# Optimization experiments

Hardware: AMD Instinct MI355X
Metric: run time of the kernel (lower is better)

Reference implementation:

```python
import jax, jax.numpy as jnp
import numpy as np

B, N, C = 4, 65536, 192
HEADS = 6
HEADC = C // HEADS
EPS = 1e-5


def _ln(x, w, b):
    # custom LayerNorm: unbiased std (ddof=1), divide by (std + eps)
    m = x.mean(-1, keepdims=True)
    s = jnp.std(x, axis=-1, keepdims=True, ddof=1)
    return w * ((x - m) / (s + EPS)) + b


def setup_inputs() -> dict:
    key = jax.random.key(0)
    ks = jax.random.split(key, 8)
    x = jax.random.normal(ks[0], (B, N, C), dtype=jnp.float32)
    # 1x1 conv weights == channel matmuls; [out_c, in_c]
    qkv_w = jax.random.normal(ks[1], (3 * C, C), dtype=jnp.float32) * 0.05
    qkv_b = jax.random.normal(ks[2], (3 * C,), dtype=jnp.float32) * 0.02
    o1_w = jax.random.normal(ks[3], (C, C), dtype=jnp.float32) * 0.05
    o1_b = jax.random.normal(ks[4], (C,), dtype=jnp.float32) * 0.02
    o2_w = jax.random.normal(ks[5], (C, C), dtype=jnp.float32) * 0.05
    o2_b = jax.random.normal(ks[6], (C,), dtype=jnp.float32) * 0.02
    kln_w = jnp.ones((HEADS, 1, HEADC), dtype=jnp.float32)
    kln_b = jnp.zeros((HEADS, 1, HEADC), dtype=jnp.float32)
    vln_w = jnp.ones((HEADS, 1, HEADC), dtype=jnp.float32)
    vln_b = jnp.zeros((HEADS, 1, HEADC), dtype=jnp.float32)
    return {"x": x, "qkv_w": qkv_w, "qkv_b": qkv_b, "o1_w": o1_w,
            "o1_b": o1_b, "o2_w": o2_w, "o2_b": o2_b,
            "kln_w": kln_w, "kln_b": kln_b, "vln_w": vln_w, "vln_b": vln_b,
            "H": 256, "W": 256}


def reference(x, qkv_w, qkv_b, o1_w, o1_b, o2_w, o2_b,
              kln_w, kln_b, vln_w, vln_b, H, W):
    b, n, c = x.shape
    heads, headc = kln_w.shape[0], kln_w.shape[-1]
    # 1x1 conv QKV projection (per-pixel linear)
    qkv = jnp.einsum('bnc,dc->bnd', x, qkv_w) + qkv_b          # [B,N,3C]
    qkv = qkv.reshape(b, n, heads, 3 * headc).transpose(0, 2, 1, 3)  # [B,h,N,3d]
    q, k, v = jnp.split(qkv, 3, axis=-1)                        # each [B,h,N,d]
    k = _ln(k, kln_w, kln_b)
    v = _ln(v, vln_w, vln_b)
    # Galerkin (softmax-free) linear attention
    kv = jnp.einsum('bhnd,bhne->bhde', k, v) / n                # [B,h,d,d]
    attn = jnp.einsum('bhnd,bhde->bhne', q, kv)                 # [B,h,N,d]
    attn = attn.transpose(0, 2, 1, 3).reshape(b, n, c)          # [B,N,C]
    ret = attn + x                                              # residual
    h = jax.nn.gelu(jnp.einsum('bnc,dc->bnd', ret, o1_w) + o1_b,
                    approximate=False)
    out = jnp.einsum('bnc,dc->bnd', h, o2_w) + o2_b + x
    return out
```

## Files before the change

### kernel.cpp

```cpp
#include <hip/hip_runtime.h>
#include <math.h>

typedef __attribute__((ext_vector_type(8)))  __bf16 bf16x8;
typedef __attribute__((ext_vector_type(16))) float  f32x16;
typedef __attribute__((ext_vector_type(4)))  float  f32x4;
typedef __attribute__((ext_vector_type(4)))  int    i32x4;
typedef __attribute__((ext_vector_type(4)))  unsigned u32x4;

union FR { bf16x8 v; u32x4 q; unsigned u[4]; };

__device__ inline f32x16 MF(bf16x8 a, bf16x8 b, f32x16 c) {
    return __builtin_amdgcn_mfma_f32_32x32x16_bf16(a, b, c, 0, 0, 0);
}
__device__ inline unsigned pk(float a, float b) {
    unsigned ua = (__builtin_bit_cast(unsigned, a) + 0x8000u) >> 16;
    unsigned ub = (__builtin_bit_cast(unsigned, b) + 0x8000u) >> 16;
    return ua | (ub << 16);
}
__device__ inline unsigned short bfr(float a) {
    return (unsigned short)((__builtin_bit_cast(unsigned, a) + 0x8000u) >> 16);
}
__device__ inline float ubf(unsigned short s) {
    return __builtin_bit_cast(float, (unsigned)s << 16);
}
__device__ inline float gelu_f(float g) {
    float z  = g * 0.70710678118654752f;
    float az = fabsf(z);
    float t  = 1.0f / (1.0f + 0.3275911f * az);
    float poly = t*(0.254829592f + t*(-0.284496736f + t*(1.421413741f +
                 t*(-1.453152027f + t*1.061405429f))));
    float er = 1.0f - poly * __expf(-az * az);
    er = (z < 0.f) ? -er : er;
    return 0.5f * g * (1.0f + er);
}

__global__ void k0_pack(const float* __restrict__ qkv_w, const float* __restrict__ qkv_b,
                        const float* __restrict__ o2w,
                        unsigned* __restrict__ wkvpk, unsigned* __restrict__ o2pk,
                        float* __restrict__ bkv)
{
    int idx = blockIdx.x * 256 + threadIdx.x;
    if (idx < 36864) {
        int kt = idx / 3072, r = idx % 3072, nt = r / 256, r3 = r % 256;
        int l = r3 >> 2, q = r3 & 3;
        int c  = kt * 16 + (l >> 5) * 8 + q * 2;
        int rp = nt * 32 + (l & 31);
        int row = (rp >> 6) * 96 + 32 + (rp & 63);
        wkvpk[idx] = pk(qkv_w[row * 192 + c], qkv_w[row * 192 + c + 1]);
    } else if (idx < 55296) {
        int i2 = idx - 36864;
        int kt = i2 / 1536, r = i2 % 1536, jt = r / 256, r3 = r % 256;
        int l = r3 >> 2, q = r3 & 3;
        int jj = kt * 16 + (l >> 5) * 8 + q * 2;
        int j  = jt * 32 + (l & 31);
        o2pk[i2] = pk(o2w[j * 192 + jj], o2w[j * 192 + jj + 1]);
    } else if (idx < 55680) {
        int rp = idx - 55296;
        bkv[rp] = qkv_b[(rp >> 6) * 96 + 32 + (rp & 63)];
    }
}

__global__ __launch_bounds__(256, 2)
void k1a(const float* __restrict__ x, const u32x4* __restrict__ Wpk,
         const float* __restrict__ bkv, u32x4* __restrict__ kvraw)
{
    const int tid = threadIdx.x;
    const int wid = tid >> 6, lane = tid & 63;
    const int col = lane & 31, lh = lane >> 5;
    const int w = blockIdx.x * 4 + wid;
    const int b = w >> 11, sp = w & 2047;

    const float* xr = x + ((long)(b * 65536 + sp * 32 + col)) * 192 + lh * 8;
    FR afr[12];
#pragma unroll
    for (int kt = 0; kt < 12; ++kt) {
        f32x4 a0 = *(const f32x4*)(xr + kt * 16);
        f32x4 a1 = *(const f32x4*)(xr + kt * 16 + 4);
        afr[kt].u[0] = pk(a0.x, a0.y); afr[kt].u[1] = pk(a0.z, a0.w);
        afr[kt].u[2] = pk(a1.x, a1.y); afr[kt].u[3] = pk(a1.z, a1.w);
    }
    float biasv[12];
#pragma unroll
    for (int nt = 0; nt < 12; ++nt) biasv[nt] = bkv[nt * 32 + col];

#pragma unroll
    for (int half = 0; half < 2; ++half) {
        f32x16 acc[6];
#pragma unroll
        for (int n = 0; n < 6; ++n) acc[n] = (f32x16)(biasv[half * 6 + n]);
#pragma unroll
        for (int kt = 0; kt < 12; ++kt) {
            bf16x8 av = afr[kt].v;
#pragma unroll
            for (int n = 0; n < 6; ++n) {
                FR bv; bv.q = Wpk[(kt * 12 + half * 6 + n) * 64 + lane];
                acc[n] = MF(av, bv.v, acc[n]);
            }
        }
#pragma unroll
        for (int n = 0; n < 6; ++n) {
            int nt = half * 6 + n;
            u32x4 lo, hi;
            lo.x = pk(acc[n][0],  acc[n][1]);  lo.y = pk(acc[n][2],  acc[n][3]);
            lo.z = pk(acc[n][4],  acc[n][5]);  lo.w = pk(acc[n][6],  acc[n][7]);
            hi.x = pk(acc[n][8],  acc[n][9]);  hi.y = pk(acc[n][10], acc[n][11]);
            hi.z = pk(acc[n][12], acc[n][13]); hi.w = pk(acc[n][14], acc[n][15]);
            long base = ((long)((b * 2048 + sp) * 12 + nt)) * 128 + lane * 2;
            kvraw[base] = lo; kvraw[base + 1] = hi;
        }
    }
}

__global__ __launch_bounds__(256, 2)
void k1b(const u32x4* __restrict__ kvraw,
         const float* __restrict__ klnw, const float* __restrict__ klnb,
         const float* __restrict__ vlnw, const float* __restrict__ vlnb,
         float* __restrict__ kvg)
{
    __shared__ __align__(16) unsigned short kvT[64 * 40];
    __shared__ float stats[4][64][2];
    __shared__ float smean[64], sinv[64];
    __shared__ float lnw_s[64], lnb_s[64];

    const int t = threadIdx.x;
    const int split = blockIdx.x, h = blockIdx.y, b = blockIdx.z;

    if (t < 32)      { lnw_s[t] = klnw[h * 32 + t];      lnb_s[t] = klnb[h * 32 + t]; }
    else if (t < 64) { lnw_s[t] = vlnw[h * 32 + t - 32]; lnb_s[t] = vlnb[h * 32 + t - 32]; }

    const int lane = t & 63;
    const int col = lane & 31, lh = lane >> 5;
    const int nt  = 2 * h + (t >> 7);
    const int l   = (t & 127) >> 1;
    const int rh  = (t & 1) * 8;
    const int chw = (t >> 7) * 32 + (l & 31);
    const int p0  = 4 * (l >> 5) + rh * 2;
    const int c64 = t & 63, pp = c64 & 31, kvh = c64 >> 5, qq = t >> 6;

    f32x16 kvacc = (f32x16)(0.0f);

    for (int c = 0; c < 32; ++c) {
        int sp = split * 32 + c;
        __syncthreads();
        u32x4 d = kvraw[((long)((b * 2048 + sp) * 12 + nt)) * 128 + l * 2 + (t & 1)];
        *(uint2*)&kvT[chw * 40 + p0]     = make_uint2(d.x, d.y);
        *(uint2*)&kvT[chw * 40 + p0 + 8] = make_uint2(d.z, d.w);
        __syncthreads();
        float vals[8]; float s = 0.f, s2 = 0.f;
#pragma unroll
        for (int i = 0; i < 8; ++i) {
            int ch = kvh * 32 + qq * 8 + i;
            float f = ubf(kvT[ch * 40 + pp]);
            vals[i] = f; s += f; s2 += f * f;
        }
        stats[qq][c64][0] = s; stats[qq][c64][1] = s2;
        __syncthreads();
        if (t < 64) {
            float ss = 0.f, ss2 = 0.f;
#pragma unroll
            for (int q = 0; q < 4; ++q) { ss += stats[q][t][0]; ss2 += stats[q][t][1]; }
            float m = ss * (1.f / 32.f);
            float var = fmaxf((ss2 - 32.f * m * m) * (1.f / 31.f), 0.f);
            smean[t] = m; sinv[t] = 1.f / (sqrtf(var) + 1e-5f);
        }
        __syncthreads();
        float m = smean[c64], inv = sinv[c64];
#pragma unroll
        for (int i = 0; i < 8; ++i) {
            int ch = kvh * 32 + qq * 8 + i;
            float f = lnw_s[ch] * ((vals[i] - m) * inv) + lnb_s[ch];
            kvT[ch * 40 + pp] = bfr(f);
        }
        __syncthreads();
        if (t < 64) {
#pragma unroll
            for (int kt2 = 0; kt2 < 2; ++kt2) {
                i32x4 ar = *(const i32x4*)&kvT[col * 40 + kt2 * 16 + lh * 8];
                i32x4 br = *(const i32x4*)&kvT[(32 + col) * 40 + kt2 * 16 + lh * 8];
                kvacc = MF(__builtin_bit_cast(bf16x8, ar),
                           __builtin_bit_cast(bf16x8, br), kvacc);
            }
        }
    }
    if (t < 64) {
#pragma unroll
        for (int r = 0; r < 16; ++r) {
            int dd = (r & 3) + 4 * lh + 8 * (r >> 2);
            atomicAdd(&kvg[((b * 6 + h) * 32 + dd) * 32 + col],
                      kvacc[r] * (1.f / 65536.f));
        }
    }
}

__global__ void k2a(const float* __restrict__ qkv_w, const float* __restrict__ qkv_b,
                    const float* __restrict__ kvg,
                    float* __restrict__ Pt, float* __restrict__ c0)
{
    int b = blockIdx.y;
    const float* kvb = kvg + (long)b * 6144;
    if (blockIdx.x < 144) {
        int idx = blockIdx.x * 256 + threadIdx.x;
        int c = idx % 192, cp = idx / 192;
        int h = cp >> 5, e = cp & 31;
        float s = 0.f;
#pragma unroll 8
        for (int d = 0; d < 32; ++d)
            s += qkv_w[(h * 96 + d) * 192 + c] * kvb[(h * 32 + d) * 32 + e];
        Pt[(long)b * 36864 + cp * 192 + c] = s;
    } else if (threadIdx.x < 192) {
        int cp = threadIdx.x, h = cp >> 5, e = cp & 31;
        float s = 0.f;
#pragma unroll 8
        for (int d = 0; d < 32; ++d)
            s += qkv_b[h * 96 + d] * kvb[(h * 32 + d) * 32 + e];
        c0[b * 192 + cp] = s;
    }
}

__global__ void k2b(const float* __restrict__ o1w, const float* __restrict__ o1b,
                    const float* __restrict__ Pt, const float* __restrict__ c0,
                    float* __restrict__ M1t, float* __restrict__ d1)
{
    int b = blockIdx.y;
    if (blockIdx.x < 144) {
        int idx = blockIdx.x * 256 + threadIdx.x;
        int c = idx % 192, j = idx / 192;
        float s = o1w[j * 192 + c];
        const float* pb = Pt + (long)b * 36864;
        const float* wr = o1w + j * 192;
#pragma unroll 8
        for (int cp = 0; cp < 192; ++cp)
            s += pb[cp * 192 + c] * wr[cp];
        M1t[(long)b * 36864 + j * 192 + c] = s;
    } else if (threadIdx.x < 192) {
        int j = threadIdx.x;
        float s = o1b[j];
        const float* wr = o1w + j * 192;
#pragma unroll 8
        for (int cp = 0; cp < 192; ++cp)
            s += c0[b * 192 + cp] * wr[cp];
        d1[b * 192 + j] = s;
    }
}

__global__ void k2c(const float* __restrict__ M1t, unsigned* __restrict__ M1pk)
{
    int idx = blockIdx.x * 256 + threadIdx.x;
    if (idx < 73728) {
        int b = idx / 18432, r = idx % 18432;
        int kt = r / 1536, r2 = r % 1536, jt = r2 / 256, r3 = r2 % 256;
        int l = r3 >> 2, q = r3 & 3;
        int c = kt * 16 + (l >> 5) * 8 + q * 2;
        int j = jt * 32 + (l & 31);
        const float* src = M1t + (long)b * 36864 + j * 192 + c;
        M1pk[idx] = pk(src[0], src[1]);
    }
}

__global__ __launch_bounds__(256, 2)
void k3(const float* __restrict__ x, const u32x4* __restrict__ M1bf,
        const float* __restrict__ d1, const u32x4* __restrict__ o2bf,
        const float* __restrict__ o2b, float* __restrict__ out)
{
    __shared__ __align__(16) unsigned short hbuf[4][32 * 200];
    const int tid = threadIdx.x;
    const int wid = tid >> 6, lane = tid & 63;
    const int col = lane & 31, lh = lane >> 5;
    const int w = blockIdx.x * 4 + wid;
    const int b = w >> 11, sp = w & 2047;

    const float* xrow = x + ((long)(b * 65536 + sp * 32)) * 192;
    const float* xr = xrow + col * 192 + lh * 8;
    FR afr[12];
#pragma unroll
    for (int kt = 0; kt < 12; ++kt) {
        f32x4 a0 = *(const f32x4*)(xr + kt * 16);
        f32x4 a1 = *(const f32x4*)(xr + kt * 16 + 4);
        afr[kt].u[0] = pk(a0.x, a0.y); afr[kt].u[1] = pk(a0.z, a0.w);
        afr[kt].u[2] = pk(a1.x, a1.y); afr[kt].u[3] = pk(a1.z, a1.w);
    }
    float d1v[6], o2bv[6];
#pragma unroll
    for (int jt = 0; jt < 6; ++jt) {
        d1v[jt]  = d1[b * 192 + jt * 32 + col];
        o2bv[jt] = o2b[jt * 32 + col];
    }

    f32x16 acc[6];
#pragma unroll
    for (int jt = 0; jt < 6; ++jt) acc[jt] = (f32x16)(d1v[jt]);
    const u32x4* W1 = M1bf + b * 4608;
#pragma unroll
    for (int kt = 0; kt < 12; ++kt) {
        bf16x8 av = afr[kt].v;
#pragma unroll
        for (int jt = 0; jt < 6; ++jt) {
            FR bv; bv.q = W1[(kt * 6 + jt) * 64 + lane];
            acc[jt] = MF(av, bv.v, acc[jt]);
        }
    }
    unsigned short* hb = hbuf[wid];
#pragma unroll
    for (int jt = 0; jt < 6; ++jt)
#pragma unroll
        for (int r = 0; r < 16; ++r) {
            int p = (r & 3) + 4 * lh + 8 * (r >> 2);
            hb[p * 200 + jt * 32 + col] = bfr(gelu_f(acc[jt][r]));
        }
    __syncthreads();
    i32x4 hfr[12];
#pragma unroll
    for (int kt = 0; kt < 12; ++kt)
        hfr[kt] = *(const i32x4*)&hb[col * 200 + kt * 16 + lh * 8];
    f32x16 acc2[6];
#pragma unroll
    for (int jt = 0; jt < 6; ++jt) acc2[jt] = (f32x16)(0.0f);
#pragma unroll
    for (int kt = 0; kt < 12; ++kt) {
        bf16x8 av = __builtin_bit_cast(bf16x8, hfr[kt]);
#pragma unroll
        for (int jt = 0; jt < 6; ++jt) {
            FR bv; bv.q = o2bf[(kt * 6 + jt) * 64 + lane];
            acc2[jt] = MF(av, bv.v, acc2[jt]);
        }
    }
    float* orow = out + ((long)(b * 65536 + sp * 32)) * 192;
#pragma unroll
    for (int jt = 0; jt < 6; ++jt) {
        int j = jt * 32 + col;
#pragma unroll
        for (int r = 0; r < 16; ++r) {
            int p = (r & 3) + 4 * lh + 8 * (r >> 2);
            orow[p * 192 + j] = acc2[jt][r] + o2bv[jt] + xrow[p * 192 + j];
        }
    }
}

extern "C" void kernel_launch(void* const* d_in, const int* in_sizes, int n_in,
                              void* d_out, int out_size, void* d_ws, size_t ws_size,
                              hipStream_t stream) {
    const float* x     = (const float*)d_in[0];
    const float* qkv_w = (const float*)d_in[1];
    const float* qkv_b = (const float*)d_in[2];
    const float* o1_w  = (const float*)d_in[3];
    const float* o1_b  = (const float*)d_in[4];
    const float* o2_w  = (const float*)d_in[5];
    const float* o2_b  = (const float*)d_in[6];
    const float* klnw  = (const float*)d_in[7];
    const float* klnb  = (const float*)d_in[8];
    const float* vlnw  = (const float*)d_in[9];
    const float* vlnb  = (const float*)d_in[10];
    float* out = (float*)d_out;
    float* ws  = (float*)d_ws;

    if (ws_size < (size_t)450432 * sizeof(float)) return;

    unsigned* wkvpk = (unsigned*)(ws);
    float*    bkv   = ws + 36864;
    float*    kvg   = ws + 37248;
    float*    Pt    = ws + 61824;
    float*    c0    = ws + 209280;
    float*    M1t   = ws + 210048;
    float*    d1    = ws + 357504;
    unsigned* M1pk  = (unsigned*)(ws + 358272);
    unsigned* o2pk  = (unsigned*)(ws + 432000);

    hipMemsetAsync(kvg, 0, 24576 * sizeof(float), stream);
    k0_pack<<<218, 256, 0, stream>>>(qkv_w, qkv_b, o2_w, wkvpk, o2pk, bkv);
    k1a<<<2048, 256, 0, stream>>>(x, (const u32x4*)wkvpk, bkv, (u32x4*)d_out);
    k1b<<<dim3(64, 6, 4), 256, 0, stream>>>((const u32x4*)d_out,
                                            klnw, klnb, vlnw, vlnb, kvg);
    k2a<<<dim3(145, 4), 256, 0, stream>>>(qkv_w, qkv_b, kvg, Pt, c0);
    k2b<<<dim3(145, 4), 256, 0, stream>>>(o1_w, o1_b, Pt, c0, M1t, d1);
    k2c<<<288, 256, 0, stream>>>(M1t, M1pk);
    k3<<<2048, 256, 0, stream>>>(x, (const u32x4*)M1pk, d1, (const u32x4*)o2pk,
                                 o2_b, out);
}
```

Before: 624.9 us.

## Fuse K/V projection, LayerNorm and KV outer product into one kernel

Merges the K/V projection kernel and the LayerNorm/KV-accumulation kernel into a single kernel. It normalizes in registers via per-wave LDS scratch and computes the per-head KV product with MFMA right away, accumulating into shared-memory partials per block. This removes the large bf16 round trip of raw K/V through global memory and the separate memset. A small reduction kernel sums the 128 partials per batch and applies the LayerNorm affine weights algebraically. The cost is heavy shared-memory atomics, lower occupancy from the larger LDS footprint, and a serial partial-sum reduction.

```diff
diff --git a/kernel.cpp b/kernel.cpp
--- a/kernel.cpp
+++ b/kernel.cpp
@@ -61,135 +61,151 @@
 }
 
 __global__ __launch_bounds__(256, 2)
-void k1a(const float* __restrict__ x, const u32x4* __restrict__ Wpk,
-         const float* __restrict__ bkv, u32x4* __restrict__ kvraw)
-{
+void k1(const float* __restrict__ x, const u32x4* __restrict__ Wpk,
+        const float* __restrict__ bkv, float* __restrict__ part)
+{
+    __shared__ __align__(16) float s1[6][16][64];
+    __shared__ float skv[12][64];
+    __shared__ __align__(16) float scr[4][64 * 34];
+    __shared__ __align__(8)  float st[4][2][32][2];
+
     const int tid = threadIdx.x;
     const int wid = tid >> 6, lane = tid & 63;
     const int col = lane & 31, lh = lane >> 5;
-    const int w = blockIdx.x * 4 + wid;
-    const int b = w >> 11, sp = w & 2047;
-
-    const float* xr = x + ((long)(b * 65536 + sp * 32 + col)) * 192 + lh * 8;
-    FR afr[12];
-#pragma unroll
-    for (int kt = 0; kt < 12; ++kt) {
-        f32x4 a0 = *(const f32x4*)(xr + kt * 16);
-        f32x4 a1 = *(const f32x4*)(xr + kt * 16 + 4);
-        afr[kt].u[0] = pk(a0.x, a0.y); afr[kt].u[1] = pk(a0.z, a0.w);
-        afr[kt].u[2] = pk(a1.x, a1.y); afr[kt].u[3] = pk(a1.z, a1.w);
-    }
-    float biasv[12];
-#pragma unroll
-    for (int nt = 0; nt < 12; ++nt) biasv[nt] = bkv[nt * 32 + col];
-
-#pragma unroll
-    for (int half = 0; half < 2; ++half) {
-        f32x16 acc[6];
-#pragma unroll
-        for (int n = 0; n < 6; ++n) acc[n] = (f32x16)(biasv[half * 6 + n]);
+    const int g = blockIdx.x, b = g >> 7, gb = g & 127;
+
+    for (int i = tid; i < 6144; i += 256) ((float*)s1)[i] = 0.f;
+    for (int i = tid; i < 768;  i += 256) ((float*)skv)[i] = 0.f;
+    __syncthreads();
+
+    float* sc  = scr[wid];
+    float* stw = (float*)st[wid];
+
+    for (int it = 0; it < 4; ++it) {
+        const int sp = gb * 16 + wid * 4 + it;
+        const float* xr = x + ((long)(b * 65536 + sp * 32 + col)) * 192 + lh * 8;
+        FR afr[12];
 #pragma unroll
         for (int kt = 0; kt < 12; ++kt) {
-            bf16x8 av = afr[kt].v;
-#pragma unroll
-            for (int n = 0; n < 6; ++n) {
-                FR bv; bv.q = Wpk[(kt * 12 + half * 6 + n) * 64 + lane];
-                acc[n] = MF(av, bv.v, acc[n]);
+            f32x4 a0 = *(const f32x4*)(xr + kt * 16);
+            f32x4 a1 = *(const f32x4*)(xr + kt * 16 + 4);
+            afr[kt].u[0] = pk(a0.x, a0.y); afr[kt].u[1] = pk(a0.z, a0.w);
+            afr[kt].u[2] = pk(a1.x, a1.y); afr[kt].u[3] = pk(a1.z, a1.w);
+        }
+
+        for (int h = 0; h < 6; ++h) {
+            f32x16 acck = (f32x16)(bkv[(2 * h) * 32 + col]);
+            f32x16 accv = (f32x16)(bkv[(2 * h + 1) * 32 + col]);
+#pragma unroll
+            for (int kt = 0; kt < 12; ++kt) {
+                FR bk_, bv_;
+                bk_.q = Wpk[(kt * 12 + 2 * h) * 64 + lane];
+                bv_.q = Wpk[(kt * 12 + 2 * h + 1) * 64 + lane];
+                acck = MF(afr[kt].v, bk_.v, acck);
+                accv = MF(afr[kt].v, bv_.v, accv);
             }
-        }
-#pragma unroll
-        for (int n = 0; n < 6; ++n) {
-            int nt = half * 6 + n;
-            u32x4 lo, hi;
-            lo.x = pk(acc[n][0],  acc[n][1]);  lo.y = pk(acc[n][2],  acc[n][3]);
-            lo.z = pk(acc[n][4],  acc[n][5]);  lo.w = pk(acc[n][6],  acc[n][7]);
-            hi.x = pk(acc[n][8],  acc[n][9]);  hi.y = pk(acc[n][10], acc[n][11]);
-            hi.z = pk(acc[n][12], acc[n][13]); hi.w = pk(acc[n][14], acc[n][15]);
-            long base = ((long)((b * 2048 + sp) * 12 + nt)) * 128 + lane * 2;
-            kvraw[base] = lo; kvraw[base + 1] = hi;
-        }
-    }
-}
-
-__global__ __launch_bounds__(256, 2)
-void k1b(const u32x4* __restrict__ kvraw,
+#pragma unroll
+            for (int r = 0; r < 16; r += 2) {
+                int p = (r & 3) + 4 * lh + 8 * (r >> 2);
+                *(float2*)&sc[col * 34 + p]        = make_float2(acck[r], acck[r + 1]);
+                *(float2*)&sc[(32 + col) * 34 + p] = make_float2(accv[r], accv[r + 1]);
+            }
+            __builtin_amdgcn_wave_barrier();
+            {
+                const float* cb = sc + (lh * 32) * 34 + col;
+                float s = 0.f, s2 = 0.f;
+#pragma unroll
+                for (int ch = 0; ch < 32; ++ch) {
+                    float v = cb[ch * 34];
+                    s += v; s2 = fmaf(v, v, s2);
+                }
+                float m   = s * (1.f / 32.f);
+                float var = fmaxf((s2 - 32.f * m * m) * (1.f / 31.f), 0.f);
+                float inv = 1.f / (sqrtf(var) + 1e-5f);
+                *(float2*)&stw[(lh * 32 + col) * 2] = make_float2(m, inv);
+            }
+            __builtin_amdgcn_wave_barrier();
+            float skl = 0.f, svl = 0.f;
+            unsigned pkk[8], pkv[8];
+#pragma unroll
+            for (int j = 0; j < 8; ++j) {
+                int r0 = 2 * j;
+                int p0 = (r0 & 3) + 4 * lh + 8 * (r0 >> 2);
+                float2 a0 = *(float2*)&stw[p0 * 2];
+                float2 a1 = *(float2*)&stw[(p0 + 1) * 2];
+                float2 c0 = *(float2*)&stw[(32 + p0) * 2];
+                float2 c1 = *(float2*)&stw[(32 + p0 + 1) * 2];
+                float k0 = (acck[r0]     - a0.x) * a0.y;
+                float k1v = (acck[r0 + 1] - a1.x) * a1.y;
+                float v0 = (accv[r0]     - c0.x) * c0.y;
+                float v1 = (accv[r0 + 1] - c1.x) * c1.y;
+                skl += k0 + k1v; svl += v0 + v1;
+                pkk[j] = pk(k0, k1v); pkv[j] = pk(v0, v1);
+            }
+            atomicAdd(&skv[h][lane], skl);
+            atomicAdd(&skv[6 + h][lane], svl);
+            unsigned ka0 = __shfl_xor((int)(lh ? pkk[0] : pkk[2]), 32);
+            unsigned ka1 = __shfl_xor((int)(lh ? pkk[1] : pkk[3]), 32);
+            unsigned ka2 = __shfl_xor((int)(lh ? pkk[4] : pkk[6]), 32);
+            unsigned ka3 = __shfl_xor((int)(lh ? pkk[5] : pkk[7]), 32);
+            unsigned vb0 = __shfl_xor((int)(lh ? pkv[0] : pkv[2]), 32);
+            unsigned vb1 = __shfl_xor((int)(lh ? pkv[1] : pkv[3]), 32);
+            unsigned vb2 = __shfl_xor((int)(lh ? pkv[4] : pkv[6]), 32);
+            unsigned vb3 = __shfl_xor((int)(lh ? pkv[5] : pkv[7]), 32);
+            FR A0, A1, B0, B1;
+            A0.u[0] = lh ? ka0 : pkk[0]; A0.u[1] = lh ? ka1 : pkk[1];
+            A0.u[2] = lh ? pkk[2] : ka0; A0.u[3] = lh ? pkk[3] : ka1;
+            A1.u[0] = lh ? ka2 : pkk[4]; A1.u[1] = lh ? ka3 : pkk[5];
+            A1.u[2] = lh ? pkk[6] : ka2; A1.u[3] = lh ? pkk[7] : ka3;
+            B0.u[0] = lh ? vb0 : pkv[0]; B0.u[1] = lh ? vb1 : pkv[1];
+            B0.u[2] = lh ? pkv[2] : vb0; B0.u[3] = lh ? pkv[3] : vb1;
+            B1.u[0] = lh ? vb2 : pkv[4]; B1.u[1] = lh ? vb3 : pkv[5];
+            B1.u[2] = lh ? pkv[6] : vb2; B1.u[3] = lh ? pkv[7] : vb3;
+            f32x16 ph = (f32x16)(0.f);
+            ph = MF(A0.v, B0.v, ph);
+            ph = MF(A1.v, B1.v, ph);
+#pragma unroll
+            for (int r = 0; r < 16; ++r) atomicAdd(&s1[h][r][lane], ph[r]);
+            __builtin_amdgcn_wave_barrier();
+        }
+    }
+    __syncthreads();
+    float* pb = part + (long)g * 6912;
+    for (int i = tid; i < 6144; i += 256) pb[i] = ((float*)s1)[i];
+    for (int i = tid; i < 768;  i += 256) pb[6144 + i] = ((float*)skv)[i];
+}
+
+__global__ __launch_bounds__(1024)
+void k1c(const float* __restrict__ part,
          const float* __restrict__ klnw, const float* __restrict__ klnb,
          const float* __restrict__ vlnw, const float* __restrict__ vlnb,
          float* __restrict__ kvg)
 {
-    __shared__ __align__(16) unsigned short kvT[64 * 40];
-    __shared__ float stats[4][64][2];
-    __shared__ float smean[64], sinv[64];
-    __shared__ float lnw_s[64], lnb_s[64];
-
+    __shared__ float sks[32], svs[32];
+    const int bh = blockIdx.x, b = bh / 6, h = bh % 6;
     const int t = threadIdx.x;
-    const int split = blockIdx.x, h = blockIdx.y, b = blockIdx.z;
-
-    if (t < 32)      { lnw_s[t] = klnw[h * 32 + t];      lnb_s[t] = klnb[h * 32 + t]; }
-    else if (t < 64) { lnw_s[t] = vlnw[h * 32 + t - 32]; lnb_s[t] = vlnb[h * 32 + t - 32]; }
-
-    const int lane = t & 63;
-    const int col = lane & 31, lh = lane >> 5;
-    const int nt  = 2 * h + (t >> 7);
-    const int l   = (t & 127) >> 1;
-    const int rh  = (t & 1) * 8;
-    const int chw = (t >> 7) * 32 + (l & 31);
-    const int p0  = 4 * (l >> 5) + rh * 2;
-    const int c64 = t & 63, pp = c64 & 31, kvh = c64 >> 5, qq = t >> 6;
-
-    f32x16 kvacc = (f32x16)(0.0f);
-
-    for (int c = 0; c < 32; ++c) {
-        int sp = split * 32 + c;
-        __syncthreads();
-        u32x4 d = kvraw[((long)((b * 2048 + sp) * 12 + nt)) * 128 + l * 2 + (t & 1)];
-        *(uint2*)&kvT[chw * 40 + p0]     = make_uint2(d.x, d.y);
-        *(uint2*)&kvT[chw * 40 + p0 + 8] = make_uint2(d.z, d.w);
-        __syncthreads();
-        float vals[8]; float s = 0.f, s2 = 0.f;
-#pragma unroll
-        for (int i = 0; i < 8; ++i) {
-            int ch = kvh * 32 + qq * 8 + i;
-            float f = ubf(kvT[ch * 40 + pp]);
-            vals[i] = f; s += f; s2 += f * f;
-        }
-        stats[qq][c64][0] = s; stats[qq][c64][1] = s2;
-        __syncthreads();
-        if (t < 64) {
-            float ss = 0.f, ss2 = 0.f;
-#pragma unroll
-            for (int q = 0; q < 4; ++q) { ss += stats[q][t][0]; ss2 += stats[q][t][1]; }
-            float m = ss * (1.f / 32.f);
-            float var = fmaxf((ss2 - 32.f * m * m) * (1.f / 31.f), 0.f);
-            smean[t] = m; sinv[t] = 1.f / (sqrtf(var) + 1e-5f);
-        }
-        __syncthreads();
-        float m = smean[c64], inv = sinv[c64];
-#pragma unroll
-        for (int i = 0; i < 8; ++i) {
-            int ch = kvh * 32 + qq * 8 + i;
-            float f = lnw_s[ch] * ((vals[i] - m) * inv) + lnb_s[ch];
-            kvT[ch * 40 + pp] = bfr(f);
-        }
-        __syncthreads();
-        if (t < 64) {
-#pragma unroll
-            for (int kt2 = 0; kt2 < 2; ++kt2) {
-                i32x4 ar = *(const i32x4*)&kvT[col * 40 + kt2 * 16 + lh * 8];
-                i32x4 br = *(const i32x4*)&kvT[(32 + col) * 40 + kt2 * 16 + lh * 8];
-                kvacc = MF(__builtin_bit_cast(bf16x8, ar),
-                           __builtin_bit_cast(bf16x8, br), kvacc);
-            }
-        }
-    }
+    const int d = t >> 5, e = t & 31;
+    const int lhd = (d >> 2) & 1, r = (d & 3) + 4 * (d >> 3);
+    const float* pb = part + (long)(b * 128) * 6912;
+    const int off = h * 1024 + r * 64 + (e + 32 * lhd);
+    float s = 0.f;
+#pragma unroll 4
+    for (int w = 0; w < 128; ++w) s += pb[(long)w * 6912 + off];
     if (t < 64) {
-#pragma unroll
-        for (int r = 0; r < 16; ++r) {
-            int dd = (r & 3) + 4 * lh + 8 * (r >> 2);
-            atomicAdd(&kvg[((b * 6 + h) * 32 + dd) * 32 + col],
-                      kvacc[r] * (1.f / 65536.f));
-        }
-    }
+        int tt = t & 31;
+        int o2 = 6144 + (t < 32 ? 0 : 384) + h * 64 + tt;
+        float acc = 0.f;
+#pragma unroll 4
+        for (int w = 0; w < 128; ++w)
+            acc += pb[(long)w * 6912 + o2] + pb[(long)w * 6912 + o2 + 32];
+        if (t < 32) sks[tt] = acc; else svs[tt] = acc;
+    }
+    __syncthreads();
+    float kw = klnw[h * 32 + d], kb = klnb[h * 32 + d];
+    float vw = vlnw[h * 32 + e], vb = vlnb[h * 32 + e];
+    float kv = (kw * vw * s + kw * vb * sks[d] + kb * vw * svs[e]) * (1.f / 65536.f)
+             + kb * vb;
+    kvg[((b * 6 + h) * 32 + d) * 32 + e] = kv;
 }
 
 __global__ void k2a(const float* __restrict__ qkv_w, const float* __restrict__ qkv_b,
@@ -365,11 +381,9 @@
     unsigned* M1pk  = (unsigned*)(ws + 358272);
     unsigned* o2pk  = (unsigned*)(ws + 432000);
 
-    hipMemsetAsync(kvg, 0, 24576 * sizeof(float), stream);
     k0_pack<<<218, 256, 0, stream>>>(qkv_w, qkv_b, o2_w, wkvpk, o2pk, bkv);
-    k1a<<<2048, 256, 0, stream>>>(x, (const u32x4*)wkvpk, bkv, (u32x4*)d_out);
-    k1b<<<dim3(64, 6, 4), 256, 0, stream>>>((const u32x4*)d_out,
-                                            klnw, klnb, vlnw, vlnb, kvg);
+    k1<<<512, 256, 0, stream>>>(x, (const u32x4*)wkvpk, bkv, (float*)d_out);
+    k1c<<<24, 1024, 0, stream>>>((const float*)d_out, klnw, klnb, vlnw, vlnb, kvg);
     k2a<<<dim3(145, 4), 256, 0, stream>>>(qkv_w, qkv_b, kvg, Pt, c0);
     k2b<<<dim3(145, 4), 256, 0, stream>>>(o1_w, o1_b, Pt, c0, M1t, d1);
     k2c<<<288, 256, 0, stream>>>(M1t, M1pk);
```

Result: slower. 764.6 us (+22.3%).
